# Kernel tuning notes

Hardware: AMD Instinct MI355X
Metric: run time of the kernel (lower is better)

## Reference

```python
import jax, jax.numpy as jnp
import numpy as np

N = 100000   # nodes
E = 1000000  # edges (before self-loops)
D_IN = 16
H, C = 2, 64  # heads, hidden per head
EPS = 1e-5    # BatchNorm eps
SLOPE = 0.2   # LeakyReLU negative slope (GATConv default)


def setup_inputs() -> dict:
    key = jax.random.key(0)
    ks = jax.random.split(key, 40)
    rn = lambda k, s, sc=0.1: jax.random.normal(k, s, jnp.float32) * sc
    inp = {}
    inp["x"] = jax.random.normal(ks[0], (N, D_IN), jnp.float32)
    inp["edge_index"] = jax.random.randint(ks[1], (2, E), 0, N)
    i = 2
    for l, din in ((1, D_IN), (2, C), (3, C)):
        inp[f"W{l}"] = rn(ks[i], (din, H * C)); i += 1
        inp[f"as{l}"] = rn(ks[i], (H, C)); i += 1
        inp[f"ad{l}"] = rn(ks[i], (H, C)); i += 1
        inp[f"b{l}"] = jnp.zeros((C,), jnp.float32)
        inp[f"g{l}"] = jnp.ones((C,), jnp.float32)   # BN gamma
        inp[f"be{l}"] = jnp.zeros((C,), jnp.float32) # BN beta
    inp["mW1"] = rn(ks[i], (C + 5, C)); i += 1
    inp["mb1"] = jnp.zeros((C,), jnp.float32)
    inp["mW2"] = rn(ks[i], (C, C)); i += 1
    inp["mb2"] = jnp.zeros((C,), jnp.float32)
    inp["pW"] = rn(ks[i], (C, 1)); i += 1
    inp["pb"] = jnp.zeros((1,), jnp.float32)
    inp["vW"] = rn(ks[i], (C, 1)); i += 1
    inp["vb"] = jnp.zeros((1,), jnp.float32)
    return inp


def gat(x, src, dst, W, att_s, att_d, bias):
    # GATConv, heads=H, concat=False (mean over heads). Messages flow src->dst.
    h = (x @ W).reshape(-1, H, C)               # [N,H,C]
    a_s = jnp.sum(h * att_s, -1)                # [N,H]
    a_d = jnp.sum(h * att_d, -1)                # [N,H]
    e = jax.nn.leaky_relu(a_s[src] + a_d[dst], SLOPE)  # [Etot,H]
    e = e - jax.ops.segment_max(e, dst, num_segments=N)[dst]
    ee = jnp.exp(e)
    alpha = ee / (jax.ops.segment_sum(ee, dst, num_segments=N)[dst] + 1e-16)
    msg = h[src] * alpha[:, :, None]            # [Etot,H,C]
    out = jax.ops.segment_sum(msg, dst, num_segments=N)  # [N,H,C]
    return out.mean(1) + bias                   # [N,C]


def bn(h, g, b):
    m = h.mean(0)
    v = jnp.mean((h - m) ** 2, 0)  # biased variance (torch BN normalization)
    return (h - m) * jax.lax.rsqrt(v + EPS) * g + b


def reference(x, edge_index, W1, as1, ad1, b1, g1, be1,
              W2, as2, ad2, b2, g2, be2, W3, as3, ad3, b3, g3, be3,
              mW1, mb1, mW2, mb2, pW, pb, vW, vb):
    loops = jnp.arange(N)
    src = jnp.concatenate([edge_index[0], loops])  # add_self_loops=True
    dst = jnp.concatenate([edge_index[1], loops])
    ctx = x[:, 9:14]  # context features [N,5]
    h = jax.nn.relu(bn(gat(x, src, dst, W1, as1, ad1, b1), g1, be1))
    h = jax.nn.relu(bn(gat(h, src, dst, W2, as2, ad2, b2), g2, be2))
    h = jax.nn.relu(bn(gat(h, src, dst, W3, as3, ad3, b3), g3, be3))
    # dropout is identity in eval reference
    h = jnp.concatenate([h, ctx], axis=1)          # [N, C+5]
    h = jax.nn.relu(h @ mW1 + mb1) @ mW2 + mb2     # MLP
    logits = (h @ pW + pb).squeeze(-1)             # [N]
    value = (h @ vW + vb).squeeze(-1)              # [N]
    return logits, value
```

## Files before the change

kernel.cpp:

```cpp
#include <hip/hip_runtime.h>
#include <hip/hip_fp16.h>


__device__ __forceinline__ float leaky(float x) { return x > 0.f ? x : 0.2f * x; }

typedef float f32x4 __attribute__((ext_vector_type(4)));

#define BCAP 4096
#define NSL 256

__global__ void bucket_hist(const int* __restrict__ dst, int* __restrict__ bcnt, int E) {
  __shared__ int cnt[512];
  int t = threadIdx.x;
  cnt[t] = 0; cnt[t + 256] = 0;
  __syncthreads();
  for (int e = blockIdx.x * blockDim.x + t; e < E; e += gridDim.x * blockDim.x)
    atomicAdd(&cnt[dst[e] >> 8], 1);
  __syncthreads();
  for (int i = t; i < 512; i += 256)
    if (cnt[i]) atomicAdd(&bcnt[i], cnt[i]);
}

__global__ void bucket_scan(const int* __restrict__ bcnt, int* __restrict__ boff,
                            int* __restrict__ bcur, int nbk) {
  __shared__ int temp[512];
  int t = threadIdx.x;
  int v = (t < nbk) ? bcnt[t] : 0;
  temp[t] = v;
  __syncthreads();
  for (int off = 1; off < 512; off <<= 1) {
    int add = (t >= off) ? temp[t - off] : 0;
    __syncthreads();
    temp[t] += add;
    __syncthreads();
  }
  if (t < nbk) {
    int ex = temp[t] - v;
    boff[t] = ex;
    bcur[t] = ex;
  }
}

__global__ __launch_bounds__(256) void bin_scatter(
    const int* __restrict__ src, const int* __restrict__ dst,
    int* __restrict__ bcur, int2* __restrict__ ebuf, int E) {
  __shared__ int cnt[512];
  __shared__ int base[512];
  int t = threadIdx.x;
  int beg = blockIdx.x * 8192;
  int end = min(E, beg + 8192);
  cnt[t] = 0; cnt[t + 256] = 0;
  __syncthreads();
  for (int e = beg + t; e < end; e += 256)
    atomicAdd(&cnt[dst[e] >> 8], 1);
  __syncthreads();
  for (int i = t; i < 512; i += 256) {
    base[i] = cnt[i] ? atomicAdd(&bcur[i], cnt[i]) : 0;
    cnt[i] = 0;
  }
  __syncthreads();
  for (int e = beg + t; e < end; e += 256) {
    int d = dst[e];
    int bk = d >> 8;
    int off = atomicAdd(&cnt[bk], 1);
    ebuf[base[bk] + off] = make_int2(src[e], d);
  }
}

__global__ __launch_bounds__(256) void bucket_sort(
    const int2* __restrict__ ebuf, const int* __restrict__ boff,
    int* __restrict__ col, int* __restrict__ row_ptr, int E, int n, int nbk) {
  __shared__ int2 eds[BCAP];
  __shared__ int dcnt[256];
  __shared__ int dbase[256];
  __shared__ int dexcl[256];
  int b = blockIdx.x, t = threadIdx.x;
  int S = boff[b];
  int Eend = (b + 1 < nbk) ? boff[b + 1] : E;
  int cnt = min(Eend - S, BCAP);
  for (int i = t; i < cnt; i += 256) eds[i] = ebuf[S + i];
  dcnt[t] = 0;
  __syncthreads();
  for (int i = t; i < cnt; i += 256) atomicAdd(&dcnt[eds[i].y & 255], 1);
  __syncthreads();
  int v = dcnt[t];
  dbase[t] = v;
  __syncthreads();
  for (int off = 1; off < 256; off <<= 1) {
    int add = (t >= off) ? dbase[t - off] : 0;
    __syncthreads();
    dbase[t] += add;
    __syncthreads();
  }
  int excl = dbase[t] - v;
  int d = (b << 8) + t;
  if (d < n) row_ptr[d] = S + excl;
  if (b == nbk - 1 && t == 0) row_ptr[n] = E;
  dcnt[t] = 0;
  dexcl[t] = excl;
  __syncthreads();
  for (int i = t; i < cnt; i += 256) {
    int2 e = eds[i];
    int dl = e.y & 255;
    int off = atomicAdd(&dcnt[dl], 1);
    col[S + dexcl[dl] + off] = e.x;
  }
}

__global__ __launch_bounds__(256) void bn_stats(const float* __restrict__ h,
                                                float* __restrict__ stats, int n) {
  __shared__ float ssum[64], ssq[64];
  int t = threadIdx.x;
  if (t < 64) { ssum[t] = 0.f; ssq[t] = 0.f; }
  __syncthreads();
  const float4* h4 = (const float4*)h;
  size_t total4 = (size_t)n * 16;
  size_t stride = (size_t)gridDim.x * blockDim.x;
  int cbase = ((int)(((size_t)blockIdx.x * blockDim.x + t) & 15)) * 4;
  float s0 = 0.f, s1 = 0.f, s2 = 0.f, s3 = 0.f;
  float q0 = 0.f, q1 = 0.f, q2 = 0.f, q3 = 0.f;
  for (size_t i = (size_t)blockIdx.x * blockDim.x + t; i < total4; i += stride) {
    float4 v = h4[i];
    s0 += v.x; q0 = fmaf(v.x, v.x, q0);
    s1 += v.y; q1 = fmaf(v.y, v.y, q1);
    s2 += v.z; q2 = fmaf(v.z, v.z, q2);
    s3 += v.w; q3 = fmaf(v.w, v.w, q3);
  }
  atomicAdd(&ssum[cbase + 0], s0); atomicAdd(&ssq[cbase + 0], q0);
  atomicAdd(&ssum[cbase + 1], s1); atomicAdd(&ssq[cbase + 1], q1);
  atomicAdd(&ssum[cbase + 2], s2); atomicAdd(&ssq[cbase + 2], q2);
  atomicAdd(&ssum[cbase + 3], s3); atomicAdd(&ssq[cbase + 3], q3);
  __syncthreads();
  if (t < 64) {
    stats[blockIdx.x * 128 + t] = ssum[t];
    stats[blockIdx.x * 128 + 64 + t] = ssq[t];
  }
}

__global__ void bn_finalize(const float* __restrict__ stats, const float* __restrict__ g,
                            const float* __restrict__ be, float* __restrict__ scsh,
                            float inv_n) {
  __shared__ float red[128];
  int t = threadIdx.x;
  int c = t & 63;
  int off = (t >> 6) * 64;
  float acc = 0.f;
  for (int b = 0; b < NSL; b++) acc += stats[b * 128 + off + c];
  red[t] = acc;
  __syncthreads();
  if (t < 64) {
    float mean = red[t] * inv_n;
    float var = red[64 + t] * inv_n - mean * mean;
    float sc = rsqrtf(var + 1e-5f) * g[t];
    scsh[t] = sc;
    scsh[64 + t] = be[t] - mean * sc;
  }
}

template <int K, bool BN>
__global__ __launch_bounds__(256) void gat_project_tiled(
    const float* __restrict__ act, const float* __restrict__ scsh,
    const float* __restrict__ W,
    const float* __restrict__ att_s, const float* __restrict__ att_d,
    __half2* __restrict__ hb, float* __restrict__ as_,
    float* __restrict__ ad_, int n) {
  constexpr int AST = K + 4;
  __shared__ float aS[64 * AST];
  __shared__ float wS[K * 128];
  __shared__ float attS[256];

  int t = threadIdx.x;
  int node0 = blockIdx.x * 64;
  int rows = min(64, n - node0);

  constexpr int AF4 = 64 * K / 4;
  for (int i = t; i < AF4; i += 256) {
    int r = i / (K / 4), kc = i % (K / 4);
    float4 v = make_float4(0.f, 0.f, 0.f, 0.f);
    if (r < rows) v = *(const float4*)&act[(size_t)(node0 + r) * K + kc * 4];
    if (BN) {
      float4 sc4 = *(const float4*)&scsh[kc * 4];
      float4 sh4 = *(const float4*)&scsh[64 + kc * 4];
      v.x = fmaxf(fmaf(v.x, sc4.x, sh4.x), 0.f);
      v.y = fmaxf(fmaf(v.y, sc4.y, sh4.y), 0.f);
      v.z = fmaxf(fmaf(v.z, sc4.z, sh4.z), 0.f);
      v.w = fmaxf(fmaf(v.w, sc4.w, sh4.w), 0.f);
    }
    *(float4*)&aS[r * AST + kc * 4] = v;
  }
  constexpr int WF4 = K * 32;
  for (int i = t; i < WF4; i += 256)
    *(float4*)&wS[i * 4] = *(const float4*)&W[i * 4];
  attS[t] = (t < 128) ? att_s[t] : att_d[t - 128];
  __syncthreads();

  int tc = t & 15, tr = t >> 4;
  int c0 = tc * 8, r0 = tr * 4;

  float acc[4][8] = {};
  for (int k = 0; k < K; k += 4) {
    float4 av[4];
    float4 wv[4][2];
#pragma unroll
    for (int i = 0; i < 4; i++) av[i] = *(const float4*)&aS[(r0 + i) * AST + k];
#pragma unroll
    for (int kk = 0; kk < 4; kk++) {
      wv[kk][0] = *(const float4*)&wS[(k + kk) * 128 + c0];
      wv[kk][1] = *(const float4*)&wS[(k + kk) * 128 + c0 + 4];
    }
#pragma unroll
    for (int i = 0; i < 4; i++) {
      const float* ai = (const float*)&av[i];
#pragma unroll
      for (int kk = 0; kk < 4; kk++) {
        const float* w0 = (const float*)&wv[kk][0];
        const float* w1 = (const float*)&wv[kk][1];
#pragma unroll
        for (int j = 0; j < 4; j++) {
          acc[i][j] = fmaf(ai[kk], w0[j], acc[i][j]);
          acc[i][4 + j] = fmaf(ai[kk], w1[j], acc[i][4 + j]);
        }
      }
    }
  }

#pragma unroll
  for (int i = 0; i < 4; i++) {
    int r = r0 + i;
    float psv = 0.f, pdv = 0.f;
#pragma unroll
    for (int j = 0; j < 8; j++) {
      psv = fmaf(acc[i][j], attS[c0 + j], psv);
      pdv = fmaf(acc[i][j], attS[128 + c0 + j], pdv);
    }
    psv += __shfl_xor(psv, 1); pdv += __shfl_xor(pdv, 1);
    psv += __shfl_xor(psv, 2); pdv += __shfl_xor(pdv, 2);
    psv += __shfl_xor(psv, 4); pdv += __shfl_xor(pdv, 4);
    if (r < rows) {
      size_t base = (size_t)(node0 + r) * 64 + (c0 >> 1);
      hb[base + 0] = __floats2half2_rn(acc[i][0], acc[i][1]);
      hb[base + 1] = __floats2half2_rn(acc[i][2], acc[i][3]);
      hb[base + 2] = __floats2half2_rn(acc[i][4], acc[i][5]);
      hb[base + 3] = __floats2half2_rn(acc[i][6], acc[i][7]);
      if (tc == 0 || tc == 8) {
        int head = tc >> 3;
        as_[(node0 + r) * 2 + head] = psv;
        ad_[(node0 + r) * 2 + head] = pdv;
      }
    }
  }
}

__device__ __forceinline__ void fma8(float* a, float my, uint4 raw) {
  float2 f;
  f = __half22float2(__builtin_bit_cast(__half2, raw.x)); a[0] = fmaf(my, f.x, a[0]); a[1] = fmaf(my, f.y, a[1]);
  f = __half22float2(__builtin_bit_cast(__half2, raw.y)); a[2] = fmaf(my, f.x, a[2]); a[3] = fmaf(my, f.y, a[3]);
  f = __half22float2(__builtin_bit_cast(__half2, raw.z)); a[4] = fmaf(my, f.x, a[4]); a[5] = fmaf(my, f.y, a[5]);
  f = __half22float2(__builtin_bit_cast(__half2, raw.w)); a[6] = fmaf(my, f.x, a[6]); a[7] = fmaf(my, f.y, a[7]);
}

__global__ __launch_bounds__(256) void gat_aggregate(
    const __half2* __restrict__ hb,
    const float* __restrict__ as_, const float* __restrict__ ad_,
    const int* __restrict__ row_ptr, const int* __restrict__ col,
    const float* __restrict__ bias, float* __restrict__ out, int n) {
  int w = (int)((blockIdx.x * blockDim.x + threadIdx.x) >> 6);
  int lane = threadIdx.x & 63;
  int g = lane >> 4, q = lane & 15;
  int d = w * 4 + g;
  if (d >= n) return;
  int hidx = (q >= 8) ? 1 : 0;
  int beg = row_ptr[d], end = row_ptr[d + 1];
  const uint4* hb4 = (const uint4*)hb;

  float ad_my = ad_[d * 2 + hidx];

  float a[8] = {};
  float asv = as_[d * 2 + hidx];
  float my = __expf(leaky(asv + ad_my));
  uint4 raw = hb4[(size_t)d * 16 + q];
  fma8(a, my, raw);
  float dpart = my;

  int k = beg;
  for (; k + 3 < end; k += 4) {
    int s0 = col[k], s1 = col[k + 1], s2 = col[k + 2], s3 = col[k + 3];
    float e0 = as_[s0 * 2 + hidx];
    float e1 = as_[s1 * 2 + hidx];
    float e2 = as_[s2 * 2 + hidx];
    float e3 = as_[s3 * 2 + hidx];
    uint4 r0 = hb4[(size_t)s0 * 16 + q];
    uint4 r1 = hb4[(size_t)s1 * 16 + q];
    uint4 r2 = hb4[(size_t)s2 * 16 + q];
    uint4 r3 = hb4[(size_t)s3 * 16 + q];
    float m0 = __expf(leaky(e0 + ad_my));
    float m1 = __expf(leaky(e1 + ad_my));
    float m2 = __expf(leaky(e2 + ad_my));
    float m3 = __expf(leaky(e3 + ad_my));
    fma8(a, m0, r0); fma8(a, m1, r1); fma8(a, m2, r2); fma8(a, m3, r3);
    dpart += m0 + m1 + m2 + m3;
  }
  for (; k < end; k++) {
    int s = col[k];
    float e = as_[s * 2 + hidx];
    uint4 r = hb4[(size_t)s * 16 + q];
    float m = __expf(leaky(e + ad_my));
    fma8(a, m, r);
    dpart += m;
  }

  float b[8];
#pragma unroll
  for (int i = 0; i < 8; i++) b[i] = __shfl_xor(a[i], 8);
  float denO = __shfl_xor(dpart, 8);

  if (q < 8) {
    float rr0 = 1.f / (dpart + 1e-16f), rr1 = 1.f / (denO + 1e-16f);
    float4 bl = *(const float4*)&bias[q * 8];
    float4 bh = *(const float4*)&bias[q * 8 + 4];
    f32x4 o0, o1;
    o0.x = 0.5f * (a[0] * rr0 + b[0] * rr1) + bl.x;
    o0.y = 0.5f * (a[1] * rr0 + b[1] * rr1) + bl.y;
    o0.z = 0.5f * (a[2] * rr0 + b[2] * rr1) + bl.z;
    o0.w = 0.5f * (a[3] * rr0 + b[3] * rr1) + bl.w;
    o1.x = 0.5f * (a[4] * rr0 + b[4] * rr1) + bh.x;
    o1.y = 0.5f * (a[5] * rr0 + b[5] * rr1) + bh.y;
    o1.z = 0.5f * (a[6] * rr0 + b[6] * rr1) + bh.z;
    o1.w = 0.5f * (a[7] * rr0 + b[7] * rr1) + bh.w;
    f32x4* outp = (f32x4*)&out[(size_t)d * 64 + q * 8];
    __builtin_nontemporal_store(o0, outp);
    __builtin_nontemporal_store(o1, outp + 1);
  }
}

__global__ __launch_bounds__(256) void mlp_head_tiled(
    const float* __restrict__ h3raw, const float* __restrict__ scsh,
    const float* __restrict__ x,
    const float* __restrict__ mW1, const float* __restrict__ mb1,
    const float* __restrict__ mW2, const float* __restrict__ mb2,
    const float* __restrict__ pW, const float* __restrict__ pb,
    const float* __restrict__ vW, const float* __restrict__ vb,
    float* __restrict__ out, int n) {
  __shared__ float lds[13632];
  float* a1  = lds;
  float* ctx = lds + 4352;
  float* a2  = lds + 4864;
  float* w1  = lds + 9216;
  float* w2  = lds;

  int t = threadIdx.x;
  int node0 = blockIdx.x * 64;
  int rows = min(64, n - node0);

#pragma unroll
  for (int i = 0; i < 4; i++) {
    int flat = t + i * 256;
    int r = flat >> 4, kc = flat & 15;
    float4 v = make_float4(0.f, 0.f, 0.f, 0.f);
    if (r < rows) v = *(const float4*)&h3raw[(size_t)(node0 + r) * 64 + kc * 4];
    float4 sc4 = *(const float4*)&scsh[kc * 4];
    float4 sh4 = *(const float4*)&scsh[64 + kc * 4];
    v.x = fmaxf(fmaf(v.x, sc4.x, sh4.x), 0.f);
    v.y = fmaxf(fmaf(v.y, sc4.y, sh4.y), 0.f);
    v.z = fmaxf(fmaf(v.z, sc4.z, sh4.z), 0.f);
    v.w = fmaxf(fmaf(v.w, sc4.w, sh4.w), 0.f);
    *(float4*)&a1[r * 68 + kc * 4] = v;
  }
  for (int i = t; i < 320; i += 256) {
    int r = i / 5, j = i % 5;
    ctx[r * 8 + j] = (r < rows) ? x[(size_t)(node0 + r) * 16 + 9 + j] : 0.f;
  }
#pragma unroll
  for (int i = 0; i < 5; i++) {
    int flat = t + i * 256;
    if (flat < 1104) *(float4*)&w1[flat * 4] = *(const float4*)&mW1[flat * 4];
  }
  __syncthreads();

  int tc = t & 15, tr = t >> 4;
  int c0 = tc * 4, r0 = tr * 4;

  float acc[4][4] = {};
  for (int k = 0; k < 64; k += 4) {
    float4 av[4], wv[4];
#pragma unroll
    for (int i = 0; i < 4; i++) av[i] = *(const float4*)&a1[(r0 + i) * 68 + k];
#pragma unroll
    for (int j = 0; j < 4; j++) wv[j] = *(const float4*)&w1[(k + j) * 64 + c0];
#pragma unroll
    for (int i = 0; i < 4; i++) {
      const float* ai = (const float*)&av[i];
#pragma unroll
      for (int kk = 0; kk < 4; kk++) {
        const float* wr = (const float*)&wv[kk];
        acc[i][0] = fmaf(ai[kk], wr[0], acc[i][0]);
        acc[i][1] = fmaf(ai[kk], wr[1], acc[i][1]);
        acc[i][2] = fmaf(ai[kk], wr[2], acc[i][2]);
        acc[i][3] = fmaf(ai[kk], wr[3], acc[i][3]);
      }
    }
  }
#pragma unroll
  for (int k = 64; k < 69; k++) {
    float4 wv = *(const float4*)&w1[k * 64 + c0];
    const float* wr = (const float*)&wv;
#pragma unroll
    for (int i = 0; i < 4; i++) {
      float a = ctx[(r0 + i) * 8 + (k - 64)];
      acc[i][0] = fmaf(a, wr[0], acc[i][0]);
      acc[i][1] = fmaf(a, wr[1], acc[i][1]);
      acc[i][2] = fmaf(a, wr[2], acc[i][2]);
      acc[i][3] = fmaf(a, wr[3], acc[i][3]);
    }
  }
  float b1v0 = mb1[c0], b1v1 = mb1[c0 + 1], b1v2 = mb1[c0 + 2], b1v3 = mb1[c0 + 3];
#pragma unroll
  for (int i = 0; i < 4; i++) {
    float4 t1;
    t1.x = fmaxf(acc[i][0] + b1v0, 0.f);
    t1.y = fmaxf(acc[i][1] + b1v1, 0.f);
    t1.z = fmaxf(acc[i][2] + b1v2, 0.f);
    t1.w = fmaxf(acc[i][3] + b1v3, 0.f);
    *(float4*)&a2[(r0 + i) * 68 + c0] = t1;
  }
  __syncthreads();

#pragma unroll
  for (int i = 0; i < 4; i++) {
    int flat = t + i * 256;
    *(float4*)&w2[flat * 4] = *(const float4*)&mW2[flat * 4];
  }
  __syncthreads();

  float acc2[4][4] = {};
  for (int k = 0; k < 64; k += 4) {
    float4 av[4], wv[4];
#pragma unroll
    for (int i = 0; i < 4; i++) av[i] = *(const float4*)&a2[(r0 + i) * 68 + k];
#pragma unroll
    for (int j = 0; j < 4; j++) wv[j] = *(const float4*)&w2[(k + j) * 64 + c0];
#pragma unroll
    for (int i = 0; i < 4; i++) {
      const float* ai = (const float*)&av[i];
#pragma unroll
      for (int kk = 0; kk < 4; kk++) {
        const float* wr = (const float*)&wv[kk];
        acc2[i][0] = fmaf(ai[kk], wr[0], acc2[i][0]);
        acc2[i][1] = fmaf(ai[kk], wr[1], acc2[i][1]);
        acc2[i][2] = fmaf(ai[kk], wr[2], acc2[i][2]);
        acc2[i][3] = fmaf(ai[kk], wr[3], acc2[i][3]);
      }
    }
  }

  float b2v[4], pwv[4], vwv[4];
#pragma unroll
  for (int j = 0; j < 4; j++) {
    b2v[j] = mb2[c0 + j];
    pwv[j] = pW[c0 + j];
    vwv[j] = vW[c0 + j];
  }
  float p[4], v[4];
#pragma unroll
  for (int i = 0; i < 4; i++) {
    float ps = 0.f, vs = 0.f;
#pragma unroll
    for (int j = 0; j < 4; j++) {
      float u = acc2[i][j] + b2v[j];
      ps = fmaf(u, pwv[j], ps);
      vs = fmaf(u, vwv[j], vs);
    }
    p[i] = ps; v[i] = vs;
  }
#pragma unroll
  for (int off = 1; off < 16; off <<= 1) {
#pragma unroll
    for (int i = 0; i < 4; i++) {
      p[i] += __shfl_xor(p[i], off);
      v[i] += __shfl_xor(v[i], off);
    }
  }
  if (tc == 0) {
    float pbs = pb[0], vbs = vb[0];
#pragma unroll
    for (int i = 0; i < 4; i++) {
      int r = r0 + i;
      if (r < rows) {
        out[node0 + r] = p[i] + pbs;
        out[n + node0 + r] = v[i] + vbs;
      }
    }
  }
}

extern "C" void kernel_launch(void* const* d_in, const int* in_sizes, int n_in,
                              void* d_out, int out_size, void* d_ws, size_t ws_size,
                              hipStream_t stream) {
  const float* x = (const float*)d_in[0];
  const int* ei = (const int*)d_in[1];
  const float* W[3]  = {(const float*)d_in[2],  (const float*)d_in[8],  (const float*)d_in[14]};
  const float* AS[3] = {(const float*)d_in[3],  (const float*)d_in[9],  (const float*)d_in[15]};
  const float* AD[3] = {(const float*)d_in[4],  (const float*)d_in[10], (const float*)d_in[16]};
  const float* B[3]  = {(const float*)d_in[5],  (const float*)d_in[11], (const float*)d_in[17]};
  const float* G[3]  = {(const float*)d_in[6],  (const float*)d_in[12], (const float*)d_in[18]};
  const float* BE[3] = {(const float*)d_in[7],  (const float*)d_in[13], (const float*)d_in[19]};
  const float* mW1 = (const float*)d_in[20];
  const float* mb1 = (const float*)d_in[21];
  const float* mW2 = (const float*)d_in[22];
  const float* mb2 = (const float*)d_in[23];
  const float* pW  = (const float*)d_in[24];
  const float* pb  = (const float*)d_in[25];
  const float* vW  = (const float*)d_in[26];
  const float* vb  = (const float*)d_in[27];

  const int N = in_sizes[0] / 16;
  const int E = in_sizes[1] / 2;
  const int* srcp = ei;
  const int* dstp = ei + E;

  float* bufB  = (float*)d_ws;
  float* hbuf  = bufB + (size_t)N * 64;
  float* as_   = hbuf + (size_t)N * 64;
  float* ad_   = as_ + (size_t)N * 2;
  float* stats = ad_ + (size_t)N * 2;
  float* scsh  = stats + NSL * 128;
  int* row_ptr = (int*)(scsh + 128);
  int* bcnt    = row_ptr + (N + 1);
  int* boff    = bcnt + 512;
  int* bcur    = boff + 512;
  int* col     = bcur + 512;
  int2* ebuf   = (int2*)(col + E);
  __half2* hb  = (__half2*)hbuf;

  const int nbk = (N + 255) >> 8;
  const float inv_n = 1.0f / (float)N;

  hipMemsetAsync(bcnt, 0, sizeof(int) * 512, stream);
  bucket_hist<<<256, 256, 0, stream>>>(dstp, bcnt, E);
  bucket_scan<<<1, 512, 0, stream>>>(bcnt, boff, bcur, nbk);
  bin_scatter<<<(E + 8191) / 8192, 256, 0, stream>>>(srcp, dstp, bcur, ebuf, E);
  bucket_sort<<<nbk, 256, 0, stream>>>(ebuf, boff, col, row_ptr, E, N, nbk);

  const int tiles = (N + 63) / 64;
  const int agg_blocks = (N + 15) / 16;

  for (int l = 0; l < 3; l++) {
    if (l == 0)
      gat_project_tiled<16, false><<<tiles, 256, 0, stream>>>(x, scsh, W[l], AS[l], AD[l],
                                                              hb, as_, ad_, N);
    else
      gat_project_tiled<64, true><<<tiles, 256, 0, stream>>>(bufB, scsh, W[l], AS[l], AD[l],
                                                             hb, as_, ad_, N);
    gat_aggregate<<<agg_blocks, 256, 0, stream>>>(hb, as_, ad_, row_ptr, col,
                                                  B[l], bufB, N);
    bn_stats<<<NSL, 256, 0, stream>>>(bufB, stats, N);
    bn_finalize<<<1, 128, 0, stream>>>(stats, G[l], BE[l], scsh, inv_n);
  }

  mlp_head_tiled<<<tiles, 256, 0, stream>>>(bufB, scsh, x, mW1, mb1, mW2, mb2,
                                            pW, pb, vW, vb, (float*)d_out, N);
}
```

Baseline: 488.3 us.

## Use fp16 MFMA for GAT projection with LDS-staged coalesced output

Replaces the scalar FP32 register-tiled projection GEMM with 16x16x32 fp16 MFMA instructions. Activations and a transposed copy of W are staged in LDS as half precision, with K padded to 32 for the first layer. Attention logits are reduced from the MFMA accumulators by cross-lane shuffles. The projected features are written through LDS so each thread stores a coalesced 16-byte chunk. This trades FP32 precision in the GEMM inputs for fewer ALU instructions, and adds extra LDS round trips and barriers.

```diff
diff --git a/kernel.cpp b/kernel.cpp
--- a/kernel.cpp
+++ b/kernel.cpp
@@ -5,6 +5,7 @@
 __device__ __forceinline__ float leaky(float x) { return x > 0.f ? x : 0.2f * x; }
 
 typedef float f32x4 __attribute__((ext_vector_type(4)));
+typedef _Float16 f16x8 __attribute__((ext_vector_type(8)));
 
 #define BCAP 4096
 #define NSL 256
@@ -158,26 +159,33 @@
 }
 
 template <int K, bool BN>
-__global__ __launch_bounds__(256) void gat_project_tiled(
+__global__ __launch_bounds__(256) void gat_project_mfma(
     const float* __restrict__ act, const float* __restrict__ scsh,
     const float* __restrict__ W,
     const float* __restrict__ att_s, const float* __restrict__ att_d,
     __half2* __restrict__ hb, float* __restrict__ as_,
     float* __restrict__ ad_, int n) {
-  constexpr int AST = K + 4;
-  __shared__ float aS[64 * AST];
-  __shared__ float wS[K * 128];
+  constexpr int KE = (K < 32) ? 32 : K;
+  constexpr int KP = KE + 8;
+  constexpr int STAGE = 64 * KP * 2 + 128 * KP * 2;
+  constexpr int HSZ = 64 * 136 * 2;
+  constexpr int LDSZ = (STAGE > HSZ) ? STAGE : HSZ;
+  __shared__ __align__(16) char ldsb[LDSZ];
   __shared__ float attS[256];
+  __half* aH = (__half*)ldsb;
+  __half* wT = (__half*)(ldsb + 64 * KP * 2);
+  __half* hS = (__half*)ldsb;
 
   int t = threadIdx.x;
   int node0 = blockIdx.x * 64;
   int rows = min(64, n - node0);
 
-  constexpr int AF4 = 64 * K / 4;
-  for (int i = t; i < AF4; i += 256) {
-    int r = i / (K / 4), kc = i % (K / 4);
+  constexpr int ACH = 64 * KE / 4;
+  for (int i = t; i < ACH; i += 256) {
+    int r = i / (KE / 4), kc = i % (KE / 4);
     float4 v = make_float4(0.f, 0.f, 0.f, 0.f);
-    if (r < rows) v = *(const float4*)&act[(size_t)(node0 + r) * K + kc * 4];
+    if (r < rows && kc * 4 < K)
+      v = *(const float4*)&act[(size_t)(node0 + r) * K + kc * 4];
     if (BN) {
       float4 sc4 = *(const float4*)&scsh[kc * 4];
       float4 sh4 = *(const float4*)&scsh[64 + kc * 4];
@@ -186,68 +194,80 @@
       v.z = fmaxf(fmaf(v.z, sc4.z, sh4.z), 0.f);
       v.w = fmaxf(fmaf(v.w, sc4.w, sh4.w), 0.f);
     }
-    *(float4*)&aS[r * AST + kc * 4] = v;
-  }
-  constexpr int WF4 = K * 32;
-  for (int i = t; i < WF4; i += 256)
-    *(float4*)&wS[i * 4] = *(const float4*)&W[i * 4];
+    __half2 h01 = __floats2half2_rn(v.x, v.y);
+    __half2 h23 = __floats2half2_rn(v.z, v.w);
+    uint2 pk = make_uint2(__builtin_bit_cast(unsigned, h01),
+                          __builtin_bit_cast(unsigned, h23));
+    *(uint2*)&aH[r * KP + kc * 4] = pk;
+  }
+  for (int i = t; i < KE * 128; i += 256) {
+    int k = i >> 7, c = i & 127;
+    float wv = (k < K) ? W[k * 128 + c] : 0.f;
+    wT[c * KP + k] = __float2half(wv);
+  }
   attS[t] = (t < 128) ? att_s[t] : att_d[t - 128];
   __syncthreads();
 
-  int tc = t & 15, tr = t >> 4;
-  int c0 = tc * 8, r0 = tr * 4;
-
-  float acc[4][8] = {};
-  for (int k = 0; k < K; k += 4) {
-    float4 av[4];
-    float4 wv[4][2];
-#pragma unroll
-    for (int i = 0; i < 4; i++) av[i] = *(const float4*)&aS[(r0 + i) * AST + k];
-#pragma unroll
-    for (int kk = 0; kk < 4; kk++) {
-      wv[kk][0] = *(const float4*)&wS[(k + kk) * 128 + c0];
-      wv[kk][1] = *(const float4*)&wS[(k + kk) * 128 + c0 + 4];
-    }
-#pragma unroll
-    for (int i = 0; i < 4; i++) {
-      const float* ai = (const float*)&av[i];
-#pragma unroll
-      for (int kk = 0; kk < 4; kk++) {
-        const float* w0 = (const float*)&wv[kk][0];
-        const float* w1 = (const float*)&wv[kk][1];
-#pragma unroll
-        for (int j = 0; j < 4; j++) {
-          acc[i][j] = fmaf(ai[kk], w0[j], acc[i][j]);
-          acc[i][4 + j] = fmaf(ai[kk], w1[j], acc[i][4 + j]);
-        }
-      }
-    }
-  }
-
+  int w = t >> 6, l = t & 63;
+  int cl = l & 15, r4 = l >> 4;
+  int w16 = w * 16;
+
+  f32x4 acc[8] = {};
+#pragma unroll
+  for (int ks = 0; ks < KE / 32; ks++) {
+    f16x8 av = *(const f16x8*)&aH[(w16 + cl) * KP + ks * 32 + r4 * 8];
+#pragma unroll
+    for (int ct = 0; ct < 8; ct++) {
+      f16x8 bv = *(const f16x8*)&wT[(ct * 16 + cl) * KP + ks * 32 + r4 * 8];
+      acc[ct] = __builtin_amdgcn_mfma_f32_16x16x32_f16(av, bv, acc[ct], 0, 0, 0);
+    }
+  }
+
+  float ats[8], atd[8];
+#pragma unroll
+  for (int ct = 0; ct < 8; ct++) {
+    ats[ct] = attS[ct * 16 + cl];
+    atd[ct] = attS[128 + ct * 16 + cl];
+  }
 #pragma unroll
   for (int i = 0; i < 4; i++) {
-    int r = r0 + i;
-    float psv = 0.f, pdv = 0.f;
-#pragma unroll
-    for (int j = 0; j < 8; j++) {
-      psv = fmaf(acc[i][j], attS[c0 + j], psv);
-      pdv = fmaf(acc[i][j], attS[128 + c0 + j], pdv);
-    }
-    psv += __shfl_xor(psv, 1); pdv += __shfl_xor(pdv, 1);
-    psv += __shfl_xor(psv, 2); pdv += __shfl_xor(pdv, 2);
-    psv += __shfl_xor(psv, 4); pdv += __shfl_xor(pdv, 4);
-    if (r < rows) {
-      size_t base = (size_t)(node0 + r) * 64 + (c0 >> 1);
-      hb[base + 0] = __floats2half2_rn(acc[i][0], acc[i][1]);
-      hb[base + 1] = __floats2half2_rn(acc[i][2], acc[i][3]);
-      hb[base + 2] = __floats2half2_rn(acc[i][4], acc[i][5]);
-      hb[base + 3] = __floats2half2_rn(acc[i][6], acc[i][7]);
-      if (tc == 0 || tc == 8) {
-        int head = tc >> 3;
-        as_[(node0 + r) * 2 + head] = psv;
-        ad_[(node0 + r) * 2 + head] = pdv;
-      }
-    }
+    float s0 = 0.f, s1 = 0.f, d0 = 0.f, d1 = 0.f;
+#pragma unroll
+    for (int ct = 0; ct < 4; ct++) {
+      s0 = fmaf(acc[ct][i], ats[ct], s0);
+      d0 = fmaf(acc[ct][i], atd[ct], d0);
+      s1 = fmaf(acc[ct + 4][i], ats[ct + 4], s1);
+      d1 = fmaf(acc[ct + 4][i], atd[ct + 4], d1);
+    }
+#pragma unroll
+    for (int off = 1; off < 16; off <<= 1) {
+      s0 += __shfl_xor(s0, off); s1 += __shfl_xor(s1, off);
+      d0 += __shfl_xor(d0, off); d1 += __shfl_xor(d1, off);
+    }
+    int rloc = w16 + r4 * 4 + i;
+    if (rloc < rows) {
+      int row = node0 + rloc;
+      if (cl == 0) as_[row * 2] = s0;
+      else if (cl == 1) as_[row * 2 + 1] = s1;
+      else if (cl == 2) ad_[row * 2] = d0;
+      else if (cl == 3) ad_[row * 2 + 1] = d1;
+    }
+  }
+
+  __syncthreads();
+#pragma unroll
+  for (int ct = 0; ct < 8; ct++)
+#pragma unroll
+    for (int i = 0; i < 4; i++)
+      hS[(w16 + r4 * 4 + i) * 136 + ct * 16 + cl] = __float2half(acc[ct][i]);
+  __syncthreads();
+#pragma unroll
+  for (int it = 0; it < 4; it++) {
+    int flat = t + it * 256;
+    int nd = flat >> 4, ch = flat & 15;
+    if (nd < rows)
+      *(uint4*)((char*)hb + (((size_t)(node0 + nd)) << 8) + (ch << 4)) =
+          *(const uint4*)((const char*)hS + nd * 272 + (ch << 4));
   }
 }
 
@@ -546,11 +566,11 @@
 
   for (int l = 0; l < 3; l++) {
     if (l == 0)
-      gat_project_tiled<16, false><<<tiles, 256, 0, stream>>>(x, scsh, W[l], AS[l], AD[l],
-                                                              hb, as_, ad_, N);
+      gat_project_mfma<16, false><<<tiles, 256, 0, stream>>>(x, scsh, W[l], AS[l], AD[l],
+                                                             hb, as_, ad_, N);
     else
-      gat_project_tiled<64, true><<<tiles, 256, 0, stream>>>(bufB, scsh, W[l], AS[l], AD[l],
-                                                             hb, as_, ad_, N);
+      gat_project_mfma<64, true><<<tiles, 256, 0, stream>>>(bufB, scsh, W[l], AS[l], AD[l],
+                                                            hb, as_, ad_, N);
     gat_aggregate<<<agg_blocks, 256, 0, stream>>>(hb, as_, ad_, row_ptr, col,
                                                   B[l], bufB, N);
     bn_stats<<<NSL, 256, 0, stream>>>(bufB, stats, N);
```

Measured after the change: 471.5 us. 1.04x faster.
